# Kernel optimization log

Measured on AMD Instinct MI355X. Metric: run time of the kernel, lower is better.

The kernel has to match this reference:

```python
import jax, jax.numpy as jnp
import numpy as np

DIM = 128
HIDDEN = 384  # int(32 * ((128*3 + 31) // 32))
B = 4
N_DATA = 100000
E = 200000
N_LOGICAL = 4096
EPS = 1e-05


def _rmsnorm(x, w):
    return x * jax.lax.rsqrt(jnp.mean(x * x, axis=-1, keepdims=True) + EPS) * w


def _ffn(x, w1, w2, w3):
    return (jax.nn.silu(x @ w1) * (x @ w3)) @ w2


def setup_inputs() -> dict:
    key = jax.random.key(0)
    ks = jax.random.split(key, 12)
    s = 0.02
    inp = {
        "v": jax.random.normal(ks[0], (B, N_DATA, DIM), dtype=jnp.float32),
        "data_src": jax.random.randint(ks[1], (E,), 0, N_DATA, dtype=jnp.int32),
        "data_dst": jax.random.randint(ks[2], (E,), 0, N_LOGICAL, dtype=jnp.int32),
        "num_logical": N_LOGICAL,
        # data_update params (RMSNorm + SwiGLU FFN)
        "rms1_w": jnp.ones((DIM,), jnp.float32),
        "w1a": jax.random.normal(ks[3], (DIM, HIDDEN), jnp.float32) * s,
        "w2a": jax.random.normal(ks[4], (HIDDEN, DIM), jnp.float32) * s,
        "w3a": jax.random.normal(ks[5], (DIM, HIDDEN), jnp.float32) * s,
        # logical_update params
        "rms2_w": jnp.ones((DIM,), jnp.float32),
        "w1b": jax.random.normal(ks[6], (DIM, HIDDEN), jnp.float32) * s,
        "w2b": jax.random.normal(ks[7], (HIDDEN, DIM), jnp.float32) * s,
        "w3b": jax.random.normal(ks[8], (DIM, HIDDEN), jnp.float32) * s,
        # out_proj (Linear(dim, 1))
        "wout": jax.random.normal(ks[9], (DIM, 1), jnp.float32) * s,
        "bout": jnp.zeros((1,), jnp.float32),
    }
    return inp


def reference(v, data_src, data_dst, num_logical, rms1_w, w1a, w2a, w3a,
              rms2_w, w1b, w2b, w3b, wout, bout):
    # v_act = tanh(data_update(v) + v)
    v_act = jnp.tanh(_ffn(_rmsnorm(v, rms1_w), w1a, w2a, w3a) + v)
    # gather data nodes, scatter-multiply into logical nodes (identity = 1)
    gathered = v_act[:, data_src, :]  # [B, E, D]
    l = jax.vmap(lambda g: jax.ops.segment_prod(g, data_dst, num_segments=num_logical))(gathered)  # [B, NL, D]
    l = _ffn(_rmsnorm(l, rms2_w), w1b, w2b, w3b) + l
    return (l @ wout + bout)[..., 0]  # [B, NL]
```

## Files before the change

kernel.cpp:

```cpp
#include <hip/hip_runtime.h>
#include <hip/hip_bf16.h>

#define DIM 128
#define HIDDEN 384
#define BATCH 4
#define NDATA 100000
#define NEDGE 200000
#define NLOG 4096

typedef __bf16 bf16x8 __attribute__((ext_vector_type(8)));
typedef __bf16 bf16x2 __attribute__((ext_vector_type(2)));
typedef float f32x4 __attribute__((ext_vector_type(4)));
typedef unsigned short u16;
typedef unsigned int u32;

__device__ __forceinline__ u16 f2bf(float f) {
  __bf16 b = (__bf16)f;
  return __builtin_bit_cast(u16, b);
}
__device__ __forceinline__ u32 pk2bf(float lo, float hi) {
  bf16x2 t;
  t[0] = (__bf16)lo;
  t[1] = (__bf16)hi;
  return __builtin_bit_cast(u32, t);
}
__device__ __forceinline__ bf16x8 as_bf(uint4 u) {
  return __builtin_bit_cast(bf16x8, u);
}
__device__ __forceinline__ float fast_tanh(float x) {
  float xc = fminf(fmaxf(x, -15.f), 15.f);
  float t = __expf(2.f * xc);
  return (t - 1.f) * __builtin_amdgcn_rcpf(t + 1.f);
}

__global__ void zero_counts_kernel(int* __restrict__ counts) {
  int i = blockIdx.x * blockDim.x + threadIdx.x;
  if (i < NLOG) counts[i] = 0;
}

__global__ void count_kernel(const int* __restrict__ dst, int* __restrict__ counts) {
  int e = blockIdx.x * blockDim.x + threadIdx.x;
  if (e < NEDGE) atomicAdd(&counts[dst[e]], 1);
}

__global__ __launch_bounds__(1024) void scan_kernel(const int* __restrict__ counts,
                                                    int* __restrict__ offsets,
                                                    int* __restrict__ cursor) {
  __shared__ int sdata[1024];
  const int t = threadIdx.x;
  const int c0 = counts[4 * t + 0];
  const int c1 = counts[4 * t + 1];
  const int c2 = counts[4 * t + 2];
  const int c3 = counts[4 * t + 3];
  const int s = c0 + c1 + c2 + c3;
  sdata[t] = s;
  __syncthreads();
  for (int off = 1; off < 1024; off <<= 1) {
    int vv = (t >= off) ? sdata[t - off] : 0;
    __syncthreads();
    sdata[t] += vv;
    __syncthreads();
  }
  const int excl = sdata[t] - s;
  const int o0 = excl, o1 = o0 + c0, o2 = o1 + c1, o3 = o2 + c2;
  offsets[4 * t + 0] = o0;
  offsets[4 * t + 1] = o1;
  offsets[4 * t + 2] = o2;
  offsets[4 * t + 3] = o3;
  cursor[4 * t + 0] = o0;
  cursor[4 * t + 1] = o1;
  cursor[4 * t + 2] = o2;
  cursor[4 * t + 3] = o3;
  if (t == 1023) offsets[NLOG] = o3 + c3;
}

__global__ void scatter_kernel(const int* __restrict__ src, const int* __restrict__ dst,
                               int* __restrict__ cursor, int* __restrict__ sorted_src) {
  int e = blockIdx.x * blockDim.x + threadIdx.x;
  if (e < NEDGE) {
    int d = dst[e];
    int pos = atomicAdd(&cursor[d], 1);
    sorted_src[pos] = src[e];
  }
}

__global__ __launch_bounds__(512) void prod_kernel_t(const float* __restrict__ va,
                                                     const int* __restrict__ offsets,
                                                     const int* __restrict__ sorted_src,
                                                     float* __restrict__ l) {
  const int s = blockIdx.x;
  const int t = threadIdx.x;
  const int beg = offsets[s];
  const int end = offsets[s + 1];
  const float* base = va + t;
  float p[8];
#pragma unroll
  for (int i = 0; i < 8; ++i) p[i] = 1.f;
  int e = beg;
  for (; e + 8 <= end; e += 8) {
#pragma unroll
    for (int i = 0; i < 8; ++i) p[i] *= base[(size_t)sorted_src[e + i] * 512];
  }
  for (; e < end; ++e) p[0] *= base[(size_t)sorted_src[e] * 512];
  const float r = ((p[0] * p[1]) * (p[2] * p[3])) * ((p[4] * p[5]) * (p[6] * p[7]));
  l[((size_t)(t >> 7) * NLOG + s) * DIM + (t & 127)] = r;
}

__global__ __launch_bounds__(256) void convert_w_kernel(
    const float* __restrict__ w1a, const float* __restrict__ w3a,
    const float* __restrict__ w2a, const float* __restrict__ w1b,
    const float* __restrict__ w3b, const float* __restrict__ w2b,
    u16* __restrict__ w1Ta, u16* __restrict__ w3Ta, u16* __restrict__ w2Ta,
    u16* __restrict__ w1Tb, u16* __restrict__ w3Tb, u16* __restrict__ w2Tb) {
  const int i = blockIdx.x * 256 + threadIdx.x;
  const int n1 = i >> 7, k1 = i & 127;
  w1Ta[i] = f2bf(w1a[k1 * HIDDEN + n1]);
  w3Ta[i] = f2bf(w3a[k1 * HIDDEN + n1]);
  w1Tb[i] = f2bf(w1b[k1 * HIDDEN + n1]);
  w3Tb[i] = f2bf(w3b[k1 * HIDDEN + n1]);
  const int n2 = i / HIDDEN, k2 = i - n2 * HIDDEN;
  w2Ta[i] = f2bf(w2a[k2 * DIM + n2]);
  w2Tb[i] = f2bf(w2b[k2 * DIM + n2]);
}

__global__ __launch_bounds__(256, 3) void ffn_mfma_kernel(
    const float* __restrict__ xin, const float* __restrict__ rmsw,
    const u16* __restrict__ w1T, const u16* __restrict__ w3T,
    const u16* __restrict__ w2T, float* __restrict__ xout, int mode) {
  __shared__ alignas(16) u16 sm[24576];
  char* const sb = (char*)sm;
  const int t = threadIdx.x;
  const int row0 = blockIdx.x * 64;

  {
    const int r = t >> 2;
    const int q = t & 3;
    const float* vr = xin + (size_t)(row0 + r) * DIM + q * 32;
    float av[32];
#pragma unroll
    for (int i = 0; i < 8; ++i) *(float4*)(av + 4 * i) = *(const float4*)(vr + 4 * i);
    float wr_[32];
#pragma unroll
    for (int i = 0; i < 8; ++i)
      *(float4*)(wr_ + 4 * i) = *(const float4*)(rmsw + q * 32 + 4 * i);
    float ss = 0.f;
#pragma unroll
    for (int i = 0; i < 32; ++i) ss += av[i] * av[i];
    ss += __shfl_xor(ss, 1);
    ss += __shfl_xor(ss, 2);
    const float scale = __builtin_amdgcn_rsqf(ss * (1.0f / DIM) + 1e-5f);
    const int r7 = r & 7;
#pragma unroll
    for (int i = 0; i < 4; ++i) {
      uint4 pk;
      pk.x = pk2bf(av[8 * i + 0] * scale * wr_[8 * i + 0],
                   av[8 * i + 1] * scale * wr_[8 * i + 1]);
      pk.y = pk2bf(av[8 * i + 2] * scale * wr_[8 * i + 2],
                   av[8 * i + 3] * scale * wr_[8 * i + 3]);
      pk.z = pk2bf(av[8 * i + 4] * scale * wr_[8 * i + 4],
                   av[8 * i + 5] * scale * wr_[8 * i + 5]);
      pk.w = pk2bf(av[8 * i + 6] * scale * wr_[8 * i + 6],
                   av[8 * i + 7] * scale * wr_[8 * i + 7]);
      const int c = q * 4 + i;
      *(uint4*)(sb + r * 256 + ((c ^ r7) << 4)) = pk;
    }
  }
  __syncthreads();

  const int wv = t >> 6;
  const int lane = t & 63;
  const int m16 = lane & 15;
  const int quad = lane >> 4;
  const int m7 = m16 & 7;

  uint4 bfr[4][4];
#pragma unroll
  for (int nt = 0; nt < 4; ++nt) {
    const int row = nt * 16 + m16;
#pragma unroll
    for (int ks = 0; ks < 4; ++ks)
      bfr[nt][ks] = *(const uint4*)(sb + row * 256 + (((4 * ks + quad) ^ m7) << 4));
  }
  __syncthreads();

  const int woff = wv * 96;
#pragma unroll 1
  for (int mt = 0; mt < 6; ++mt) {
    const size_t wrow = (size_t)(woff + mt * 16 + m16) * DIM + quad * 8;
    uint4 a1[4], a3[4];
#pragma unroll
    for (int ks = 0; ks < 4; ++ks) {
      a1[ks] = *(const uint4*)(w1T + wrow + ks * 32);
      a3[ks] = *(const uint4*)(w3T + wrow + ks * 32);
    }
    f32x4 acc1[4] = {{0.f, 0.f, 0.f, 0.f}, {0.f, 0.f, 0.f, 0.f},
                     {0.f, 0.f, 0.f, 0.f}, {0.f, 0.f, 0.f, 0.f}};
    f32x4 acc3[4] = {{0.f, 0.f, 0.f, 0.f}, {0.f, 0.f, 0.f, 0.f},
                     {0.f, 0.f, 0.f, 0.f}, {0.f, 0.f, 0.f, 0.f}};
#pragma unroll
    for (int ks = 0; ks < 4; ++ks) {
      const bf16x8 fa1 = as_bf(a1[ks]);
      const bf16x8 fa3 = as_bf(a3[ks]);
#pragma unroll
      for (int nt = 0; nt < 4; ++nt) {
        const bf16x8 fb = as_bf(bfr[nt][ks]);
        acc1[nt] = __builtin_amdgcn_mfma_f32_16x16x32_bf16(fa1, fb, acc1[nt], 0, 0, 0);
        acc3[nt] = __builtin_amdgcn_mfma_f32_16x16x32_bf16(fa3, fb, acc3[nt], 0, 0, 0);
      }
    }
    const int hch = (woff + mt * 16) >> 3;
    const int chu = (hch + (quad >> 1));
    const int half = (quad & 1) * 8;
#pragma unroll
    for (int nt = 0; nt < 4; ++nt) {
      const int row = nt * 16 + m16;
      float g[4];
#pragma unroll
      for (int r = 0; r < 4; ++r) {
        const float h1 = acc1[nt][r], h3 = acc3[nt][r];
        g[r] = h1 * __builtin_amdgcn_rcpf(1.0f + __expf(-h1)) * h3;
      }
      uint2 pk;
      pk.x = pk2bf(g[0], g[1]);
      pk.y = pk2bf(g[2], g[3]);
      *(uint2*)(sb + row * 768 + ((chu ^ m7) << 4) + half) = pk;
    }
  }
  __syncthreads();

#pragma unroll 1
  for (int mt = 0; mt < 2; ++mt) {
    const size_t wrow = (size_t)(wv * 32 + mt * 16 + m16) * HIDDEN + quad * 8;
    uint4 aw[12];
#pragma unroll
    for (int ks = 0; ks < 12; ++ks) aw[ks] = *(const uint4*)(w2T + wrow + ks * 32);
#pragma unroll 1
    for (int nt = 0; nt < 4; ++nt) {
      const int row = nt * 16 + m16;
      uint4 bg[12];
#pragma unroll
      for (int ks = 0; ks < 12; ++ks)
        bg[ks] = *(const uint4*)(sb + row * 768 + (((4 * ks + quad) ^ m7) << 4));
      f32x4 acc = {0.f, 0.f, 0.f, 0.f};
#pragma unroll
      for (int ks = 0; ks < 12; ++ks)
        acc = __builtin_amdgcn_mfma_f32_16x16x32_bf16(as_bf(aw[ks]), as_bf(bg[ks]), acc,
                                                      0, 0, 0);
      const int grow = row0 + row;
      const int d0 = wv * 32 + mt * 16 + quad * 4;
      const float4 res = *(const float4*)(xin + (size_t)grow * DIM + d0);
      float4 o;
      o.x = acc[0] + res.x;
      o.y = acc[1] + res.y;
      o.z = acc[2] + res.z;
      o.w = acc[3] + res.w;
      if (mode) {
        o.x = fast_tanh(o.x);
        o.y = fast_tanh(o.y);
        o.z = fast_tanh(o.z);
        o.w = fast_tanh(o.w);
        const int b = grow / NDATA;
        const int i = grow - b * NDATA;
        *(float4*)(xout + ((size_t)i * BATCH + b) * DIM + d0) = o;
      } else {
        *(float4*)(xout + (size_t)grow * DIM + d0) = o;
      }
    }
  }
}

__global__ __launch_bounds__(256) void readout_kernel(const float* __restrict__ fbuf,
                                                      const float* __restrict__ wout,
                                                      const float* __restrict__ bout,
                                                      float* __restrict__ out) {
  const int t = threadIdx.x;
  const int row = blockIdx.x * 4 + (t >> 6);
  const int lane = t & 63;
  const float2 f = *(const float2*)(fbuf + (size_t)row * DIM + lane * 2);
  const float2 w = *(const float2*)(wout + lane * 2);
  float s = f.x * w.x + f.y * w.y;
  s += __shfl_xor(s, 1);
  s += __shfl_xor(s, 2);
  s += __shfl_xor(s, 4);
  s += __shfl_xor(s, 8);
  s += __shfl_xor(s, 16);
  s += __shfl_xor(s, 32);
  if (lane == 0) out[row] = s + bout[0];
}

extern "C" void kernel_launch(void* const* d_in, const int* in_sizes, int n_in,
                              void* d_out, int out_size, void* d_ws, size_t ws_size,
                              hipStream_t stream) {
  const float* v = (const float*)d_in[0];
  const int* data_src = (const int*)d_in[1];
  const int* data_dst = (const int*)d_in[2];
  const float* rms1_w = (const float*)d_in[4];
  const float* w1a = (const float*)d_in[5];
  const float* w2a = (const float*)d_in[6];
  const float* w3a = (const float*)d_in[7];
  const float* rms2_w = (const float*)d_in[8];
  const float* w1b = (const float*)d_in[9];
  const float* w2b = (const float*)d_in[10];
  const float* w3b = (const float*)d_in[11];
  const float* wout = (const float*)d_in[12];
  const float* bout = (const float*)d_in[13];
  float* out = (float*)d_out;

  char* ws = (char*)d_ws;
  size_t off = 0;
  auto take = [&](size_t bytes) -> char* {
    char* p = ws + off;
    off += (bytes + 255) & ~(size_t)255;
    return p;
  };
  float* v_act_t = (float*)take((size_t)BATCH * NDATA * DIM * 4);
  float* lbuf = (float*)take((size_t)BATCH * NLOG * DIM * 4);
  float* fbuf = (float*)take((size_t)BATCH * NLOG * DIM * 4);
  int* counts = (int*)take(NLOG * 4);
  int* offsets = (int*)take((NLOG + 1) * 4);
  int* cursor = (int*)take(NLOG * 4);
  int* sorted_src = (int*)take(NEDGE * 4);
  u16* w1Ta = (u16*)take(HIDDEN * DIM * 2);
  u16* w3Ta = (u16*)take(HIDDEN * DIM * 2);
  u16* w2Ta = (u16*)take(HIDDEN * DIM * 2);
  u16* w1Tb = (u16*)take(HIDDEN * DIM * 2);
  u16* w3Tb = (u16*)take(HIDDEN * DIM * 2);
  u16* w2Tb = (u16*)take(HIDDEN * DIM * 2);

  convert_w_kernel<<<(HIDDEN * DIM) / 256, 256, 0, stream>>>(
      w1a, w3a, w2a, w1b, w3b, w2b, w1Ta, w3Ta, w2Ta, w1Tb, w3Tb, w2Tb);
  zero_counts_kernel<<<(NLOG + 255) / 256, 256, 0, stream>>>(counts);
  count_kernel<<<(NEDGE + 255) / 256, 256, 0, stream>>>(data_dst, counts);
  scan_kernel<<<1, 1024, 0, stream>>>(counts, offsets, cursor);
  scatter_kernel<<<(NEDGE + 255) / 256, 256, 0, stream>>>(data_src, data_dst, cursor,
                                                          sorted_src);
  ffn_mfma_kernel<<<(BATCH * NDATA) / 64, 256, 0, stream>>>(v, rms1_w, w1Ta, w3Ta, w2Ta,
                                                            v_act_t, 1);
  prod_kernel_t<<<NLOG, 512, 0, stream>>>(v_act_t, offsets, sorted_src, lbuf);
  ffn_mfma_kernel<<<(BATCH * NLOG) / 64, 256, 0, stream>>>(lbuf, rms2_w, w1Tb, w3Tb, w2Tb,
                                                           fbuf, 0);
  readout_kernel<<<(BATCH * NLOG) / 4, 256, 0, stream>>>(fbuf, wout, bout, out);
}
```

Baseline: 672.0 us.

## Split FFN block into two 32-row halves to shrink LDS and vectorize prod

```diff
diff --git a/kernel.cpp b/kernel.cpp
--- a/kernel.cpp
+++ b/kernel.cpp
@@ -84,26 +84,32 @@
   }
 }
 
-__global__ __launch_bounds__(512) void prod_kernel_t(const float* __restrict__ va,
+__global__ __launch_bounds__(128) void prod_kernel_t(const float* __restrict__ va,
                                                      const int* __restrict__ offsets,
                                                      const int* __restrict__ sorted_src,
                                                      float* __restrict__ l) {
   const int s = blockIdx.x;
-  const int t = threadIdx.x;
+  const int c = threadIdx.x;
   const int beg = offsets[s];
   const int end = offsets[s + 1];
-  const float* base = va + t;
-  float p[8];
-#pragma unroll
-  for (int i = 0; i < 8; ++i) p[i] = 1.f;
+  const float* base = va + 4 * c;
+  f32x4 p[8];
+#pragma unroll
+  for (int i = 0; i < 8; ++i) p[i] = {1.f, 1.f, 1.f, 1.f};
   int e = beg;
   for (; e + 8 <= end; e += 8) {
 #pragma unroll
-    for (int i = 0; i < 8; ++i) p[i] *= base[(size_t)sorted_src[e + i] * 512];
-  }
-  for (; e < end; ++e) p[0] *= base[(size_t)sorted_src[e] * 512];
-  const float r = ((p[0] * p[1]) * (p[2] * p[3])) * ((p[4] * p[5]) * (p[6] * p[7]));
-  l[((size_t)(t >> 7) * NLOG + s) * DIM + (t & 127)] = r;
+    for (int i = 0; i < 8; ++i) {
+      const f32x4 r = *(const f32x4*)(base + (size_t)sorted_src[e + i] * 512);
+      p[i] *= r;
+    }
+  }
+  for (; e < end; ++e) {
+    const f32x4 r = *(const f32x4*)(base + (size_t)sorted_src[e] * 512);
+    p[0] *= r;
+  }
+  const f32x4 r = ((p[0] * p[1]) * (p[2] * p[3])) * ((p[4] * p[5]) * (p[6] * p[7]));
+  *(f32x4*)(l + ((size_t)(c >> 5) * NLOG + s) * DIM + (c & 31) * 4) = r;
 }
 
 __global__ __launch_bounds__(256) void convert_w_kernel(
@@ -123,11 +129,11 @@
   w2Tb[i] = f2bf(w2b[k2 * DIM + n2]);
 }
 
-__global__ __launch_bounds__(256, 3) void ffn_mfma_kernel(
+__global__ __launch_bounds__(256, 4) void ffn_mfma_kernel(
     const float* __restrict__ xin, const float* __restrict__ rmsw,
     const u16* __restrict__ w1T, const u16* __restrict__ w3T,
     const u16* __restrict__ w2T, float* __restrict__ xout, int mode) {
-  __shared__ alignas(16) u16 sm[24576];
+  __shared__ alignas(16) u16 sm[16384];
   char* const sb = (char*)sm;
   const int t = threadIdx.x;
   const int row0 = blockIdx.x * 64;
@@ -150,6 +156,7 @@
     ss += __shfl_xor(ss, 2);
     const float scale = __builtin_amdgcn_rsqf(ss * (1.0f / DIM) + 1e-5f);
     const int r7 = r & 7;
+    char* const xrow = (r < 32) ? (sb + r * 256) : (sb + 24576 + (r - 32) * 256);
 #pragma unroll
     for (int i = 0; i < 4; ++i) {
       uint4 pk;
@@ -162,7 +169,7 @@
       pk.w = pk2bf(av[8 * i + 6] * scale * wr_[8 * i + 6],
                    av[8 * i + 7] * scale * wr_[8 * i + 7]);
       const int c = q * 4 + i;
-      *(uint4*)(sb + r * 256 + ((c ^ r7) << 4)) = pk;
+      *(uint4*)(xrow + ((c ^ r7) << 4)) = pk;
     }
   }
   __syncthreads();
@@ -172,100 +179,103 @@
   const int m16 = lane & 15;
   const int quad = lane >> 4;
   const int m7 = m16 & 7;
-
-  uint4 bfr[4][4];
-#pragma unroll
-  for (int nt = 0; nt < 4; ++nt) {
-    const int row = nt * 16 + m16;
-#pragma unroll
-    for (int ks = 0; ks < 4; ++ks)
-      bfr[nt][ks] = *(const uint4*)(sb + row * 256 + (((4 * ks + quad) ^ m7) << 4));
-  }
-  __syncthreads();
-
   const int woff = wv * 96;
+
 #pragma unroll 1
-  for (int mt = 0; mt < 6; ++mt) {
-    const size_t wrow = (size_t)(woff + mt * 16 + m16) * DIM + quad * 8;
-    uint4 a1[4], a3[4];
-#pragma unroll
-    for (int ks = 0; ks < 4; ++ks) {
-      a1[ks] = *(const uint4*)(w1T + wrow + ks * 32);
-      a3[ks] = *(const uint4*)(w3T + wrow + ks * 32);
-    }
-    f32x4 acc1[4] = {{0.f, 0.f, 0.f, 0.f}, {0.f, 0.f, 0.f, 0.f},
-                     {0.f, 0.f, 0.f, 0.f}, {0.f, 0.f, 0.f, 0.f}};
-    f32x4 acc3[4] = {{0.f, 0.f, 0.f, 0.f}, {0.f, 0.f, 0.f, 0.f},
-                     {0.f, 0.f, 0.f, 0.f}, {0.f, 0.f, 0.f, 0.f}};
-#pragma unroll
-    for (int ks = 0; ks < 4; ++ks) {
-      const bf16x8 fa1 = as_bf(a1[ks]);
-      const bf16x8 fa3 = as_bf(a3[ks]);
-#pragma unroll
-      for (int nt = 0; nt < 4; ++nt) {
-        const bf16x8 fb = as_bf(bfr[nt][ks]);
-        acc1[nt] = __builtin_amdgcn_mfma_f32_16x16x32_bf16(fa1, fb, acc1[nt], 0, 0, 0);
-        acc3[nt] = __builtin_amdgcn_mfma_f32_16x16x32_bf16(fa3, fb, acc3[nt], 0, 0, 0);
+  for (int h = 0; h < 2; ++h) {
+    const char* const xbase = (h == 0) ? sb : (sb + 24576);
+    uint4 bfr[2][4];
+#pragma unroll
+    for (int np = 0; np < 2; ++np) {
+      const int rl = np * 16 + m16;
+#pragma unroll
+      for (int ks = 0; ks < 4; ++ks)
+        bfr[np][ks] = *(const uint4*)(xbase + rl * 256 + (((4 * ks + quad) ^ m7) << 4));
+    }
+    if (h == 0) __syncthreads();
+
+#pragma unroll 1
+    for (int mt = 0; mt < 6; ++mt) {
+      const size_t wrow = (size_t)(woff + mt * 16 + m16) * DIM + quad * 8;
+      uint4 a1[4], a3[4];
+#pragma unroll
+      for (int ks = 0; ks < 4; ++ks) {
+        a1[ks] = *(const uint4*)(w1T + wrow + ks * 32);
+        a3[ks] = *(const uint4*)(w3T + wrow + ks * 32);
       }
-    }
-    const int hch = (woff + mt * 16) >> 3;
-    const int chu = (hch + (quad >> 1));
-    const int half = (quad & 1) * 8;
-#pragma unroll
-    for (int nt = 0; nt < 4; ++nt) {
-      const int row = nt * 16 + m16;
-      float g[4];
-#pragma unroll
-      for (int r = 0; r < 4; ++r) {
-        const float h1 = acc1[nt][r], h3 = acc3[nt][r];
-        g[r] = h1 * __builtin_amdgcn_rcpf(1.0f + __expf(-h1)) * h3;
+      f32x4 acc1[2] = {{0.f, 0.f, 0.f, 0.f}, {0.f, 0.f, 0.f, 0.f}};
+      f32x4 acc3[2] = {{0.f, 0.f, 0.f, 0.f}, {0.f, 0.f, 0.f, 0.f}};
+#pragma unroll
+      for (int ks = 0; ks < 4; ++ks) {
+        const bf16x8 fa1 = as_bf(a1[ks]);
+        const bf16x8 fa3 = as_bf(a3[ks]);
+#pragma unroll
+        for (int np = 0; np < 2; ++np) {
+          const bf16x8 fb = as_bf(bfr[np][ks]);
+          acc1[np] = __builtin_amdgcn_mfma_f32_16x16x32_bf16(fa1, fb, acc1[np], 0, 0, 0);
+          acc3[np] = __builtin_amdgcn_mfma_f32_16x16x32_bf16(fa3, fb, acc3[np], 0, 0, 0);
+        }
       }
-      uint2 pk;
-      pk.x = pk2bf(g[0], g[1]);
-      pk.y = pk2bf(g[2], g[3]);
-      *(uint2*)(sb + row * 768 + ((chu ^ m7) << 4) + half) = pk;
-    }
-  }
-  __syncthreads();
+      const int hch = (woff + mt * 16) >> 3;
+      const int chu = (hch + (quad >> 1));
+      const int hf = (quad & 1) * 8;
+#pragma unroll
+      for (int np = 0; np < 2; ++np) {
+        const int rl = np * 16 + m16;
+        float g[4];
+#pragma unroll
+        for (int r = 0; r < 4; ++r) {
+          const float h1 = acc1[np][r], h3 = acc3[np][r];
+          g[r] = h1 * __builtin_amdgcn_rcpf(1.0f + __expf(-h1)) * h3;
+        }
+        uint2 pk;
+        pk.x = pk2bf(g[0], g[1]);
+        pk.y = pk2bf(g[2], g[3]);
+        *(uint2*)(sb + rl * 768 + ((chu ^ m7) << 4) + hf) = pk;
+      }
+    }
+    __syncthreads();
 
 #pragma unroll 1
-  for (int mt = 0; mt < 2; ++mt) {
-    const size_t wrow = (size_t)(wv * 32 + mt * 16 + m16) * HIDDEN + quad * 8;
-    uint4 aw[12];
-#pragma unroll
-    for (int ks = 0; ks < 12; ++ks) aw[ks] = *(const uint4*)(w2T + wrow + ks * 32);
+    for (int mt = 0; mt < 2; ++mt) {
+      const size_t wrow = (size_t)(wv * 32 + mt * 16 + m16) * HIDDEN + quad * 8;
+      uint4 aw[12];
+#pragma unroll
+      for (int ks = 0; ks < 12; ++ks) aw[ks] = *(const uint4*)(w2T + wrow + ks * 32);
 #pragma unroll 1
-    for (int nt = 0; nt < 4; ++nt) {
-      const int row = nt * 16 + m16;
-      uint4 bg[12];
-#pragma unroll
-      for (int ks = 0; ks < 12; ++ks)
-        bg[ks] = *(const uint4*)(sb + row * 768 + (((4 * ks + quad) ^ m7) << 4));
-      f32x4 acc = {0.f, 0.f, 0.f, 0.f};
-#pragma unroll
-      for (int ks = 0; ks < 12; ++ks)
-        acc = __builtin_amdgcn_mfma_f32_16x16x32_bf16(as_bf(aw[ks]), as_bf(bg[ks]), acc,
-                                                      0, 0, 0);
-      const int grow = row0 + row;
-      const int d0 = wv * 32 + mt * 16 + quad * 4;
-      const float4 res = *(const float4*)(xin + (size_t)grow * DIM + d0);
-      float4 o;
-      o.x = acc[0] + res.x;
-      o.y = acc[1] + res.y;
-      o.z = acc[2] + res.z;
-      o.w = acc[3] + res.w;
-      if (mode) {
-        o.x = fast_tanh(o.x);
-        o.y = fast_tanh(o.y);
-        o.z = fast_tanh(o.z);
-        o.w = fast_tanh(o.w);
-        const int b = grow / NDATA;
-        const int i = grow - b * NDATA;
-        *(float4*)(xout + ((size_t)i * BATCH + b) * DIM + d0) = o;
-      } else {
-        *(float4*)(xout + (size_t)grow * DIM + d0) = o;
+      for (int np = 0; np < 2; ++np) {
+        const int rl = np * 16 + m16;
+        uint4 bg[12];
+#pragma unroll
+        for (int ks = 0; ks < 12; ++ks)
+          bg[ks] = *(const uint4*)(sb + rl * 768 + (((4 * ks + quad) ^ m7) << 4));
+        f32x4 acc = {0.f, 0.f, 0.f, 0.f};
+#pragma unroll
+        for (int ks = 0; ks < 12; ++ks)
+          acc = __builtin_amdgcn_mfma_f32_16x16x32_bf16(as_bf(aw[ks]), as_bf(bg[ks]),
+                                                        acc, 0, 0, 0);
+        const int grow = row0 + 32 * h + rl;
+        const int d0 = wv * 32 + mt * 16 + quad * 4;
+        const float4 res = *(const float4*)(xin + (size_t)grow * DIM + d0);
+        float4 o;
+        o.x = acc[0] + res.x;
+        o.y = acc[1] + res.y;
+        o.z = acc[2] + res.z;
+        o.w = acc[3] + res.w;
+        if (mode) {
+          o.x = fast_tanh(o.x);
+          o.y = fast_tanh(o.y);
+          o.z = fast_tanh(o.z);
+          o.w = fast_tanh(o.w);
+          const int b = grow / NDATA;
+          const int i = grow - b * NDATA;
+          *(float4*)(xout + ((size_t)i * BATCH + b) * DIM + d0) = o;
+        } else {
+          *(float4*)(xout + (size_t)grow * DIM + d0) = o;
+        }
       }
     }
+    __syncthreads();
   }
 }
 
@@ -336,7 +346,7 @@
                                                           sorted_src);
   ffn_mfma_kernel<<<(BATCH * NDATA) / 64, 256, 0, stream>>>(v, rms1_w, w1Ta, w3Ta, w2Ta,
                                                             v_act_t, 1);
-  prod_kernel_t<<<NLOG, 512, 0, stream>>>(v_act_t, offsets, sorted_src, lbuf);
+  prod_kernel_t<<<NLOG, 128, 0, stream>>>(v_act_t, offsets, sorted_src, lbuf);
   ffn_mfma_kernel<<<(BATCH * NLOG) / 64, 256, 0, stream>>>(lbuf, rms2_w, w1Tb, w3Tb, w2Tb,
                                                            fbuf, 0);
   readout_kernel<<<(BATCH * NLOG) / 4, 256, 0, stream>>>(fbuf, wout, bout, out);
```

After: 863.2 us. 28.5% more time.

## Store activated data nodes as bf16 and vectorize gather-product loads

Applied to the files above, without the earlier changes.

```diff
diff --git a/kernel.cpp b/kernel.cpp
--- a/kernel.cpp
+++ b/kernel.cpp
@@ -84,26 +84,61 @@
   }
 }
 
-__global__ __launch_bounds__(512) void prod_kernel_t(const float* __restrict__ va,
+__device__ __forceinline__ void prod_accum(uint4 u, f32x4& plo, f32x4& phi) {
+  f32x4 lo, hi;
+  lo[0] = __uint_as_float(u.x << 16);
+  lo[1] = __uint_as_float(u.x & 0xffff0000u);
+  lo[2] = __uint_as_float(u.y << 16);
+  lo[3] = __uint_as_float(u.y & 0xffff0000u);
+  hi[0] = __uint_as_float(u.z << 16);
+  hi[1] = __uint_as_float(u.z & 0xffff0000u);
+  hi[2] = __uint_as_float(u.w << 16);
+  hi[3] = __uint_as_float(u.w & 0xffff0000u);
+  plo *= lo;
+  phi *= hi;
+}
+
+__global__ __launch_bounds__(128) void prod_kernel_t(const u16* __restrict__ va,
                                                      const int* __restrict__ offsets,
                                                      const int* __restrict__ sorted_src,
                                                      float* __restrict__ l) {
   const int s = blockIdx.x;
-  const int t = threadIdx.x;
+  const int c = threadIdx.x;
   const int beg = offsets[s];
   const int end = offsets[s + 1];
-  const float* base = va + t;
-  float p[8];
-#pragma unroll
-  for (int i = 0; i < 8; ++i) p[i] = 1.f;
+  const u16* base = va + 8 * c;
+  f32x4 plo[8], phi[8];
+#pragma unroll
+  for (int i = 0; i < 8; ++i) {
+    plo[i] = {1.f, 1.f, 1.f, 1.f};
+    phi[i] = {1.f, 1.f, 1.f, 1.f};
+  }
   int e = beg;
+  for (; e < end && (e & 3); ++e) {
+    const uint4 u = *(const uint4*)(base + (size_t)sorted_src[e] * 512);
+    prod_accum(u, plo[0], phi[0]);
+  }
   for (; e + 8 <= end; e += 8) {
-#pragma unroll
-    for (int i = 0; i < 8; ++i) p[i] *= base[(size_t)sorted_src[e + i] * 512];
-  }
-  for (; e < end; ++e) p[0] *= base[(size_t)sorted_src[e] * 512];
-  const float r = ((p[0] * p[1]) * (p[2] * p[3])) * ((p[4] * p[5]) * (p[6] * p[7]));
-  l[((size_t)(t >> 7) * NLOG + s) * DIM + (t & 127)] = r;
+    const int4 ia = *(const int4*)(sorted_src + e);
+    const int4 ib = *(const int4*)(sorted_src + e + 4);
+    const int idx[8] = {ia.x, ia.y, ia.z, ia.w, ib.x, ib.y, ib.z, ib.w};
+    uint4 r[8];
+#pragma unroll
+    for (int i = 0; i < 8; ++i) r[i] = *(const uint4*)(base + (size_t)idx[i] * 512);
+#pragma unroll
+    for (int i = 0; i < 8; ++i) prod_accum(r[i], plo[i], phi[i]);
+  }
+  for (; e < end; ++e) {
+    const uint4 u = *(const uint4*)(base + (size_t)sorted_src[e] * 512);
+    prod_accum(u, plo[0], phi[0]);
+  }
+  const f32x4 rlo =
+      ((plo[0] * plo[1]) * (plo[2] * plo[3])) * ((plo[4] * plo[5]) * (plo[6] * plo[7]));
+  const f32x4 rhi =
+      ((phi[0] * phi[1]) * (phi[2] * phi[3])) * ((phi[4] * phi[5]) * (phi[6] * phi[7]));
+  float* outp = l + ((size_t)(c >> 4) * NLOG + s) * DIM + (c & 15) * 8;
+  *(f32x4*)outp = rlo;
+  *(f32x4*)(outp + 4) = rhi;
 }
 
 __global__ __launch_bounds__(256) void convert_w_kernel(
@@ -261,7 +296,11 @@
         o.w = fast_tanh(o.w);
         const int b = grow / NDATA;
         const int i = grow - b * NDATA;
-        *(float4*)(xout + ((size_t)i * BATCH + b) * DIM + d0) = o;
+        u16* const xb = (u16*)xout;
+        uint2 pk;
+        pk.x = pk2bf(o.x, o.y);
+        pk.y = pk2bf(o.z, o.w);
+        *(uint2*)(xb + ((size_t)i * BATCH + b) * DIM + d0) = pk;
       } else {
         *(float4*)(xout + (size_t)grow * DIM + d0) = o;
       }
@@ -313,7 +352,7 @@
     off += (bytes + 255) & ~(size_t)255;
     return p;
   };
-  float* v_act_t = (float*)take((size_t)BATCH * NDATA * DIM * 4);
+  u16* v_act_t = (u16*)take((size_t)BATCH * NDATA * DIM * 2);
   float* lbuf = (float*)take((size_t)BATCH * NLOG * DIM * 4);
   float* fbuf = (float*)take((size_t)BATCH * NLOG * DIM * 4);
   int* counts = (int*)take(NLOG * 4);
@@ -334,10 +373,10 @@
   scan_kernel<<<1, 1024, 0, stream>>>(counts, offsets, cursor);
   scatter_kernel<<<(NEDGE + 255) / 256, 256, 0, stream>>>(data_src, data_dst, cursor,
                                                           sorted_src);
-  ffn_mfma_kernel<<<(BATCH * NDATA) / 64, 256, 0, stream>>>(v, rms1_w, w1Ta, w3Ta, w2Ta,
-                                                            v_act_t, 1);
-  prod_kernel_t<<<NLOG, 512, 0, stream>>>(v_act_t, offsets, sorted_src, lbuf);
-  ffn_mfma_kernel<<<(BATCH * NLOG) / 64, 256, 0, stream>>>(lbuf, rms2_w, w1Tb, w3Tb, w2Tb,
-                                                           fbuf, 0);
+  ffn_mfma_kernel<<<(BATCH * NDATA) / 64, 256, 0, stream>>>(
+      v, rms1_w, w1Ta, w3Ta, w2Ta, (float*)v_act_t, 1);
+  prod_kernel_t<<<NLOG, 128, 0, stream>>>(v_act_t, offsets, sorted_src, lbuf);
+  ffn_mfma_kernel<<<(BATCH * NLOG) / 64, 256, 0, stream>>>(lbuf, rms2_w, w1Tb, w3Tb,
+                                                           w2Tb, fbuf, 0);
   readout_kernel<<<(BATCH * NLOG) / 4, 256, 0, stream>>>(fbuf, wout, bout, out);
 }
```

Measured after the change: 650.7 us. -3.2%, faster.
